# Performance work log

Hardware: AMD Instinct MI355X
Metric: run time of the kernel (lower is better)

## Reference

```python
import jax, jax.numpy as jnp
import numpy as np

N = 100000      # nodes
E = 1600000     # edges
D_IN = 64       # input feature dim
H = 64          # hidden dim
HNUM = 128      # number of direct virtual nodes (blocks)
NCONV = 2       # layers-1 conv layers in module_list
NMLP = 2        # layers-1 virtual-node MLPs (all applied each conv iter)
NEG_SLOPE = 0.2


def setup_inputs() -> dict:
    key = jax.random.key(0)
    ks = jax.random.split(key, 16)
    s = 0.1
    inp = {
        "x": jax.random.normal(ks[0], (N, D_IN), jnp.float32),
        "edge_index": jax.random.randint(ks[1], (2, E), 0, N, dtype=jnp.int32),
        "h_blocks": jax.random.randint(ks[2], (N,), 0, HNUM, dtype=jnp.int32),
        "h_levels": jax.random.randint(ks[3], (N,), 0, 4, dtype=jnp.int32),
        "h_num": HNUM,
        # initial GATConv(input->hidden): lin weight (no bias), att_src, att_dst, out bias
        "W0": jax.random.normal(ks[4], (D_IN, H), jnp.float32) * s,
        "a_src0": jax.random.normal(ks[5], (H,), jnp.float32) * s,
        "a_dst0": jax.random.normal(ks[6], (H,), jnp.float32) * s,
        "b0": jnp.zeros((H,), jnp.float32),
        # stacked module_list GATConv(hidden->hidden) params
        "Wl": jax.random.normal(ks[7], (NCONV, H, H), jnp.float32) * s,
        "a_srcl": jax.random.normal(ks[8], (NCONV, H), jnp.float32) * s,
        "a_dstl": jax.random.normal(ks[9], (NCONV, H), jnp.float32) * s,
        "bl": jnp.zeros((NCONV, H), jnp.float32),
        # virtual node embedding, torch init constant 0
        "vn_emb": jnp.zeros((1, H), jnp.float32),
        # virtual-node MLPs: Linear->ReLU->Linear->ReLU, weights stored (in,out)
        "mlp_W1": jax.random.normal(ks[10], (NMLP, H, H), jnp.float32) * s,
        "mlp_b1": jnp.zeros((NMLP, H), jnp.float32),
        "mlp_W2": jax.random.normal(ks[11], (NMLP, H, H), jnp.float32) * s,
        "mlp_b2": jnp.zeros((NMLP, H), jnp.float32),
    }
    return inp


def gat_conv(x, src, dst, W, a_src, a_dst, b, n_nodes):
    """PyG GATConv, heads=1, concat, add_self_loops=True, negative_slope=0.2."""
    h = x @ W                                    # [N, H]
    loop = jnp.arange(n_nodes, dtype=src.dtype)
    s = jnp.concatenate([src, loop])             # [E+N]
    d = jnp.concatenate([dst, loop])
    a_s = h @ a_src                              # [N]
    a_d = h @ a_dst
    e = jax.nn.leaky_relu(a_s[s] + a_d[d], negative_slope=NEG_SLOPE)  # [E+N]
    # segment softmax over destination nodes (self loops cover every segment)
    m = jax.ops.segment_max(e, d, num_segments=n_nodes)
    w = jnp.exp(e - m[d])
    denom = jax.ops.segment_sum(w, d, num_segments=n_nodes)
    alpha = w / (denom[d] + 1e-16)               # [E+N]
    out = jax.ops.segment_sum(h[s] * alpha[:, None], d, num_segments=n_nodes)
    return out + b


def reference(x, edge_index, h_blocks, h_levels, h_num,
              W0, a_src0, a_dst0, b0, Wl, a_srcl, a_dstl, bl,
              vn_emb, mlp_W1, mlp_b1, mlp_W2, mlp_b2):
    src, dst = edge_index[0], edge_index[1]
    n_nodes = x.shape[0]
    out = gat_conv(x, src, dst, W0, a_src0, a_dst0, b0, n_nodes)
    # embedding lookup of all-zero indices == broadcast of row 0
    vn_direct = jnp.broadcast_to(vn_emb[0], (h_num, vn_emb.shape[1]))  # [HNUM, H]
    vn_root = vn_emb                                                   # [1, H]
    for l in range(NCONV):
        out = out + vn_direct[h_blocks]
        out = gat_conv(out, src, dst, Wl[l], a_srcl[l], a_dstl[l], bl[l], n_nodes)
        vn_direct = jax.ops.segment_sum(out, h_blocks, num_segments=h_num) + vn_direct
        vn_direct = vn_direct + vn_root
        vn_root = jnp.sum(vn_direct, axis=0, keepdims=True) + vn_root
        # NB: the original applies EVERY vn-MLP inside each conv iteration
        for j in range(NMLP):
            vn_direct = jax.nn.relu(jax.nn.relu(vn_direct @ mlp_W1[j] + mlp_b1[j]) @ mlp_W2[j] + mlp_b2[j])
            vn_root = jax.nn.relu(jax.nn.relu(vn_root @ mlp_W1[j] + mlp_b1[j]) @ mlp_W2[j] + mlp_b2[j])
    return out
```

## Files before the change

kernel.cpp:

```cpp
#include <hip/hip_runtime.h>
#include <hip/hip_fp16.h>
#include <math.h>

#define HD 64
#define HNUM 128
#define NMLP 2
#define BSH 8
#define MAXNB 512
#define EPB 4096

typedef unsigned int uint_t;
typedef unsigned short ushort_t;
typedef _Float16 h8 __attribute__((ext_vector_type(8)));
typedef float vf4 __attribute__((ext_vector_type(4)));

union H8U { h8 v; uint_t u[4]; };

__device__ __forceinline__ float lrelu(float x){ return fmaxf(x, 0.2f*x); }

__device__ __forceinline__ float cvt_h(uint_t wv, uint_t sh){
    __half_raw hr; hr.x = (ushort_t)(wv >> sh);
    return __half2float((__half)hr);
}
__device__ __forceinline__ uint_t pk2(float a, float b){
    return (uint_t)__half_as_ushort(__float2half_rn(a)) |
           ((uint_t)__half_as_ushort(__float2half_rn(b)) << 16);
}

__global__ __launch_bounds__(256) void k_bcnt(const int* __restrict__ dst, int* __restrict__ gb,
                                              int E, int NB){
    __shared__ int h[MAXNB];
    int t = threadIdx.x;
    for(int i=t;i<NB;i+=256) h[i] = 0;
    __syncthreads();
    for(int e = blockIdx.x*256 + t; e < E; e += gridDim.x*256)
        atomicAdd(&h[dst[e]>>BSH], 1);
    __syncthreads();
    for(int i=t;i<NB;i+=256) if(h[i]) atomicAdd(&gb[i], h[i]);
}

__global__ __launch_bounds__(512) void k_bscan(const int* __restrict__ gb, int* __restrict__ bbase,
                                               int* __restrict__ gcur, int NB){
    __shared__ int s[512];
    int t = threadIdx.x;
    int v = (t < NB) ? gb[t] : 0;
    s[t] = v; __syncthreads();
    for(int o=1;o<512;o<<=1){
        int u = (t >= o) ? s[t-o] : 0;
        __syncthreads();
        s[t] += u;
        __syncthreads();
    }
    if(t < NB){ int ex = s[t] - v; bbase[t] = ex; gcur[t] = ex; }
}

__global__ __launch_bounds__(256) void k_bin(const int* __restrict__ src, const int* __restrict__ dst,
                                             int* __restrict__ gcur, uint_t* __restrict__ bdata,
                                             int E, int NB){
    __shared__ int cnt[MAXNB];
    __shared__ int base[MAXNB];
    int t = threadIdx.x;
    for(int i=t;i<NB;i+=256) cnt[i] = 0;
    __syncthreads();
    int s0 = blockIdx.x*EPB;
    uint_t pk[16]; int bk[16], off[16];
    #pragma unroll
    for(int i=0;i<16;i++){
        int e = s0 + i*256 + t;
        if(e < E){
            int sv = src[e], dv = dst[e];
            pk[i]  = ((uint_t)sv << 8) | (uint_t)(dv & 255);
            bk[i]  = dv >> BSH;
            off[i] = atomicAdd(&cnt[bk[i]], 1);
        }
    }
    __syncthreads();
    for(int i=t;i<NB;i+=256) base[i] = cnt[i] ? atomicAdd(&gcur[i], cnt[i]) : 0;
    __syncthreads();
    #pragma unroll
    for(int i=0;i<16;i++){
        int e = s0 + i*256 + t;
        if(e < E) bdata[base[bk[i]] + off[i]] = pk[i];
    }
}

__global__ __launch_bounds__(256) void k_bfuse(const uint_t* __restrict__ bdata, const int* __restrict__ bbase,
                                               const int* __restrict__ gb, int* __restrict__ rp,
                                               int* __restrict__ col, int n, int NB, int E){
    __shared__ int h[256];
    __shared__ int sc[256];
    int b = blockIdx.x, t = threadIdx.x;
    int beg = bbase[b], cnt = gb[b];
    h[t] = 0; __syncthreads();
    for(int i=t;i<cnt;i+=256) atomicAdd(&h[bdata[beg+i] & 255], 1);
    __syncthreads();
    int v = h[t];
    sc[t] = v; __syncthreads();
    for(int o=1;o<256;o<<=1){
        int u = (t >= o) ? sc[t-o] : 0;
        __syncthreads();
        sc[t] += u;
        __syncthreads();
    }
    int excl = sc[t] - v;
    int node = (b<<BSH) + t;
    if(node < n) rp[node] = beg + excl;
    if(b == NB-1 && t == 255) rp[n] = E;
    __syncthreads();
    sc[t] = excl;
    __syncthreads();
    for(int i=t;i<cnt;i+=256){
        uint_t e = bdata[beg+i];
        int pos = atomicAdd(&sc[e & 255], 1);
        col[beg + pos] = (int)(e >> 8);
    }
}

__global__ __launch_bounds__(256) void k_vcnt(const int* __restrict__ hb, int* __restrict__ vcnt, int n){
    __shared__ int h[HNUM];
    int t = threadIdx.x;
    if(t < HNUM) h[t] = 0;
    __syncthreads();
    for(int i = blockIdx.x*256 + t; i < n; i += gridDim.x*256) atomicAdd(&h[hb[i]], 1);
    __syncthreads();
    if(t < HNUM && h[t]) atomicAdd(&vcnt[t], h[t]);
}

__global__ __launch_bounds__(128) void k_vscan(const int* __restrict__ vcnt, int* __restrict__ vrp,
                                               int* __restrict__ vcur, int n){
    __shared__ int s[HNUM];
    int t = threadIdx.x;
    int v = vcnt[t];
    s[t] = v; __syncthreads();
    for(int o=1;o<HNUM;o<<=1){
        int u = (t >= o) ? s[t-o] : 0;
        __syncthreads();
        s[t] += u;
        __syncthreads();
    }
    int ex = s[t] - v;
    vrp[t] = ex; vcur[t] = ex;
    if(t == HNUM-1) vrp[HNUM] = n;
}

__global__ __launch_bounds__(256) void k_vbin(const int* __restrict__ hb, int* __restrict__ vcur,
                                              int* __restrict__ perm, int n){
    __shared__ int cnt[HNUM];
    __shared__ int base[HNUM];
    int t = threadIdx.x;
    if(t < HNUM) cnt[t] = 0;
    __syncthreads();
    int s0 = blockIdx.x*2048;
    int hv[8], off[8];
    #pragma unroll
    for(int i=0;i<8;i++){
        int nd = s0 + i*256 + t;
        if(nd < n){ hv[i] = hb[nd]; off[i] = atomicAdd(&cnt[hv[i]], 1); }
    }
    __syncthreads();
    if(t < HNUM) base[t] = cnt[t] ? atomicAdd(&vcur[t], cnt[t]) : 0;
    __syncthreads();
    #pragma unroll
    for(int i=0;i<8;i++){
        int nd = s0 + i*256 + t;
        if(nd < n) perm[base[hv[i]] + off[i]] = nd;
    }
}

__global__ __launch_bounds__(256) void k_wcvt(
    const float* __restrict__ W0, const float* __restrict__ as0, const float* __restrict__ ad0,
    const float* __restrict__ Wl, const float* __restrict__ asl, const float* __restrict__ adl,
    uint4* __restrict__ Wf3, float* __restrict__ waf3)
{
    __shared__ float wa[2][64];
    int L = blockIdx.x, t = threadIdx.x;
    const float* W  = (L==0) ? W0  : Wl  + (L-1)*HD*HD;
    const float* as = (L==0) ? as0 : asl + (L-1)*HD;
    const float* ad = (L==0) ? ad0 : adl + (L-1)*HD;
    if(t < 128){
        int sd = t>>6, k = t&63;
        const float* av = sd ? ad : as;
        float acc = 0.f;
        for(int c=0;c<HD;c++) acc = fmaf(W[k*HD+c], av[c], acc);
        wa[sd][k] = acc;
    }
    __syncthreads();
    for(int it = t; it < 512; it += 256){
        int lane = it&63, s = (it>>6)&1, tile = it>>7;
        int g = lane>>4, m = lane&15, c = tile*16 + m;
        ushort_t h[8];
        #pragma unroll
        for(int i=0;i<8;i++){
            int k = s*32 + g*4 + (i&3) + 16*(i>>2);
            h[i] = __half_as_ushort(__float2half_rn(W[k*HD + c]));
        }
        uint4 q;
        q.x = (uint_t)h[0] | ((uint_t)h[1]<<16);
        q.y = (uint_t)h[2] | ((uint_t)h[3]<<16);
        q.z = (uint_t)h[4] | ((uint_t)h[5]<<16);
        q.w = (uint_t)h[6] | ((uint_t)h[7]<<16);
        Wf3[(size_t)L*512 + (tile*2+s)*64 + lane] = q;
    }
    if(t < 128){
        int lane = t&63, sd = t>>6, g = lane>>4;
        #pragma unroll
        for(int j4=0;j4<4;j4++){
            float v[4];
            #pragma unroll
            for(int e=0;e<4;e++){
                int j = j4*4 + e;
                int k = (j>>3)*32 + g*4 + (j&3) + 16*((j>>2)&1);
                v[e] = wa[sd][k];
            }
            float* dstp = waf3 + ((size_t)L*8 + sd*4 + j4)*64*4 + lane*4;
            dstp[0]=v[0]; dstp[1]=v[1]; dstp[2]=v[2]; dstp[3]=v[3];
        }
    }
}

__global__ __launch_bounds__(256) void k_gemm(
    const float* __restrict__ IN, const float* __restrict__ addrow,
    const float* __restrict__ addtab, const int* __restrict__ hb,
    const uint4* __restrict__ Wf, const float* __restrict__ waf,
    uint_t* __restrict__ Hw, float* __restrict__ AS, float* __restrict__ AD,
    int n)
{
    __shared__ ushort_t sx[4][1024];
    int t = threadIdx.x, lane = t&63, wv = t>>6;
    int g = lane>>4, m = lane&15;
    ushort_t* sb = sx[wv];

    H8U B[8];
    #pragma unroll
    for(int f=0; f<8; f++){
        uint4 q = Wf[f*64 + lane];
        B[f].u[0]=q.x; B[f].u[1]=q.y; B[f].u[2]=q.z; B[f].u[3]=q.w;
    }
    vf4 wS[4], wD[4];
    #pragma unroll
    for(int j4=0;j4<4;j4++){
        const float* ps = waf + ((size_t)0*4 + j4)*256 + lane*4;
        const float* pd = waf + ((size_t)1*4 + j4)*256 + lane*4;
        wS[j4] = vf4{ps[0],ps[1],ps[2],ps[3]};
        wD[j4] = vf4{pd[0],pd[1],pd[2],pd[3]};
    }
    float ar0=0,ar1=0,ar2=0,ar3=0;
    if(addrow){
        const float* a = &addrow[m*4];
        ar0=a[0]; ar1=a[1]; ar2=a[2]; ar3=a[3];
    }

    int ntiles = (n + 15) >> 4;
    int wgid = (blockIdx.x*256 + t) >> 6;
    int nw = gridDim.x*4;
    for(int tile = wgid; tile < ntiles; tile += nw){
        int rb = tile*16;
        #pragma unroll
        for(int p=0;p<4;p++){
            int row = p*4 + g;
            int rowc = min(rb + row, n-1);
            float4 x4 = *(const float4*)&IN[(size_t)rowc*HD + m*4];
            if(addrow){ x4.x+=ar0; x4.y+=ar1; x4.z+=ar2; x4.w+=ar3; }
            if(addtab){
                int b = hb[rowc];
                float4 a4 = *(const float4*)&addtab[b*HD + m*4];
                x4.x+=a4.x; x4.y+=a4.y; x4.z+=a4.z; x4.w+=a4.w;
            }
            uint2 pq; pq.x = pk2(x4.x, x4.y); pq.y = pk2(x4.z, x4.w);
            int idx = (row*64 + m*4) ^ ((row&7)<<3);
            *(uint2*)&sb[idx] = pq;
        }
        int xr = (m&7)<<3;
        H8U A0, A1;
        {
            uint2 c0 = *(uint2*)&sb[(m*64 +  0 + g*4) ^ xr];
            uint2 c1 = *(uint2*)&sb[(m*64 + 16 + g*4) ^ xr];
            A0.u[0]=c0.x; A0.u[1]=c0.y; A0.u[2]=c1.x; A0.u[3]=c1.y;
            uint2 c2 = *(uint2*)&sb[(m*64 + 32 + g*4) ^ xr];
            uint2 c3 = *(uint2*)&sb[(m*64 + 48 + g*4) ^ xr];
            A1.u[0]=c2.x; A1.u[1]=c2.y; A1.u[2]=c3.x; A1.u[3]=c3.y;
        }
        float t1 = 0.f, t2 = 0.f;
        #pragma unroll
        for(int i=0;i<8;i++){
            float xv = (float)A0.v[i];
            t1 = fmaf(xv, wS[i>>2][i&3], t1);
            t2 = fmaf(xv, wD[i>>2][i&3], t2);
        }
        #pragma unroll
        for(int i=0;i<8;i++){
            float xv = (float)A1.v[i];
            t1 = fmaf(xv, wS[2+(i>>2)][i&3], t1);
            t2 = fmaf(xv, wD[2+(i>>2)][i&3], t2);
        }
        t1 += __shfl_xor(t1, 16, 64); t1 += __shfl_xor(t1, 32, 64);
        t2 += __shfl_xor(t2, 16, 64); t2 += __shfl_xor(t2, 32, 64);
        if(lane < 16 && rb + lane < n){ AS[rb+lane] = t1; AD[rb+lane] = t2; }
        vf4 z = {0.f,0.f,0.f,0.f};
        vf4 a0 = __builtin_amdgcn_mfma_f32_16x16x32_f16(A0.v, B[0].v, z, 0,0,0);
        a0     = __builtin_amdgcn_mfma_f32_16x16x32_f16(A1.v, B[1].v, a0, 0,0,0);
        vf4 a1 = __builtin_amdgcn_mfma_f32_16x16x32_f16(A0.v, B[2].v, z, 0,0,0);
        a1     = __builtin_amdgcn_mfma_f32_16x16x32_f16(A1.v, B[3].v, a1, 0,0,0);
        vf4 a2 = __builtin_amdgcn_mfma_f32_16x16x32_f16(A0.v, B[4].v, z, 0,0,0);
        a2     = __builtin_amdgcn_mfma_f32_16x16x32_f16(A1.v, B[5].v, a2, 0,0,0);
        vf4 a3 = __builtin_amdgcn_mfma_f32_16x16x32_f16(A0.v, B[6].v, z, 0,0,0);
        a3     = __builtin_amdgcn_mfma_f32_16x16x32_f16(A1.v, B[7].v, a3, 0,0,0);
        #pragma unroll
        for(int rr=0;rr<4;rr++){
            int row = rb + g*4 + rr;
            if(row < n){
                Hw[(size_t)row*32 + m]      = pk2(a0[rr], a1[rr]);
                Hw[(size_t)row*32 + 16 + m] = pk2(a2[rr], a3[rr]);
            }
        }
    }
}

__global__ __launch_bounds__(256) void k_agg(
    const uint_t* __restrict__ Hb, const float* __restrict__ AS, const float* __restrict__ AD,
    const int* __restrict__ rp, const int* __restrict__ col,
    const float* __restrict__ bias, float* __restrict__ OUT, int n)
{
    int t = threadIdx.x, lane = t & 63;
    int p = lane & 15;
    int qb = lane & 48;
    int w0 = 2*p;
    int c00 = 32*(w0>>4)+(w0&15), c01 = c00+16;
    int c10 = c00+1, c11 = c00+17;
    float b00 = bias[c00], b01 = bias[c01], b10 = bias[c10], b11 = bias[c11];
    int wv  = (blockIdx.x*256 + t) >> 6;
    int nwv = gridDim.x*4;
    for(int base = wv*4; base < n; base += nwv*4){
        int dq = min(base + (qb>>4), n-1);
        float ad = AD[dq];
        float wself = __expf(lrelu(AS[dq] + ad));
        uint2 hd = *(const uint2*)&Hb[(size_t)dq*32 + w0];
        float4 acc;
        acc.x = cvt_h(hd.x,0)*wself; acc.y = cvt_h(hd.x,16)*wself;
        acc.z = cvt_h(hd.y,0)*wself; acc.w = cvt_h(hd.y,16)*wself;
        float sacc = 0.f;
        int beg = rp[dq], end = rp[dq+1];
        int cnt = end - beg;
        int nit = (cnt + 15) >> 4;
        nit = max(nit, __shfl_xor(nit, 16, 64));
        nit = max(nit, __shfl_xor(nit, 32, 64));
        for(int it = 0; it < nit; it++){
            int j = beg + it*16 + p;
            bool valid = j < end;
            int sj = dq;
            if(cnt > 0) sj = col[valid ? j : end - 1];
            float wj = 0.f;
            if(valid) wj = __expf(lrelu(AS[sj] + ad));
            sacc += wj;
            int ccnt = cnt - it*16;
            ccnt = ccnt < 0 ? 0 : (ccnt > 16 ? 16 : ccnt);
            int emax = ccnt;
            emax = max(emax, __shfl_xor(emax, 16, 64));
            emax = max(emax, __shfl_xor(emax, 32, 64));
            int e = 0;
            for(; e + 4 <= emax; e += 4){
                float wq0 = __shfl(wj, qb+e,   64);
                float wq1 = __shfl(wj, qb+e+1, 64);
                float wq2 = __shfl(wj, qb+e+2, 64);
                float wq3 = __shfl(wj, qb+e+3, 64);
                int   sq0 = __shfl(sj, qb+e,   64);
                int   sq1 = __shfl(sj, qb+e+1, 64);
                int   sq2 = __shfl(sj, qb+e+2, 64);
                int   sq3 = __shfl(sj, qb+e+3, 64);
                uint2 v0 = *(const uint2*)&Hb[(size_t)sq0*32 + w0];
                uint2 v1 = *(const uint2*)&Hb[(size_t)sq1*32 + w0];
                uint2 v2 = *(const uint2*)&Hb[(size_t)sq2*32 + w0];
                uint2 v3 = *(const uint2*)&Hb[(size_t)sq3*32 + w0];
                acc.x = fmaf(wq0, cvt_h(v0.x,0),  acc.x);
                acc.y = fmaf(wq0, cvt_h(v0.x,16), acc.y);
                acc.z = fmaf(wq0, cvt_h(v0.y,0),  acc.z);
                acc.w = fmaf(wq0, cvt_h(v0.y,16), acc.w);
                acc.x = fmaf(wq1, cvt_h(v1.x,0),  acc.x);
                acc.y = fmaf(wq1, cvt_h(v1.x,16), acc.y);
                acc.z = fmaf(wq1, cvt_h(v1.y,0),  acc.z);
                acc.w = fmaf(wq1, cvt_h(v1.y,16), acc.w);
                acc.x = fmaf(wq2, cvt_h(v2.x,0),  acc.x);
                acc.y = fmaf(wq2, cvt_h(v2.x,16), acc.y);
                acc.z = fmaf(wq2, cvt_h(v2.y,0),  acc.z);
                acc.w = fmaf(wq2, cvt_h(v2.y,16), acc.w);
                acc.x = fmaf(wq3, cvt_h(v3.x,0),  acc.x);
                acc.y = fmaf(wq3, cvt_h(v3.x,16), acc.y);
                acc.z = fmaf(wq3, cvt_h(v3.y,0),  acc.z);
                acc.w = fmaf(wq3, cvt_h(v3.y,16), acc.w);
            }
            for(; e < emax; e++){
                float wq = __shfl(wj, qb+e, 64);
                int   sq = __shfl(sj, qb+e, 64);
                uint2 v = *(const uint2*)&Hb[(size_t)sq*32 + w0];
                acc.x = fmaf(wq, cvt_h(v.x,0),  acc.x);
                acc.y = fmaf(wq, cvt_h(v.x,16), acc.y);
                acc.z = fmaf(wq, cvt_h(v.y,0),  acc.z);
                acc.w = fmaf(wq, cvt_h(v.y,16), acc.w);
            }
        }
        sacc += __shfl_xor(sacc, 1, 64);
        sacc += __shfl_xor(sacc, 2, 64);
        sacc += __shfl_xor(sacc, 4, 64);
        sacc += __shfl_xor(sacc, 8, 64);
        float s = wself + sacc;
        float inv = 1.f/(s + 1e-16f);
        if(base + (qb>>4) < n){
            OUT[(size_t)dq*HD + c00] = fmaf(acc.x, inv, b00);
            OUT[(size_t)dq*HD + c01] = fmaf(acc.y, inv, b01);
            OUT[(size_t)dq*HD + c10] = fmaf(acc.z, inv, b10);
            OUT[(size_t)dq*HD + c11] = fmaf(acc.w, inv, b11);
        }
    }
}

__global__ __launch_bounds__(256) void k_vsum(const float* __restrict__ OUT, const int* __restrict__ perm,
                                              const int* __restrict__ vrp, float* __restrict__ vnS){
    int t = threadIdx.x, lane = t & 63, w = t >> 6;
    int g = blockIdx.x >> 3, sub = blockIdx.x & 7;
    int wig = sub*4 + w;
    int beg = vrp[g], end = vrp[g+1];
    float a0=0.f, a1=0.f, a2=0.f, a3=0.f;
    int i = beg + wig;
    for(; i + 96 < end; i += 128){
        int p0 = perm[i], p1 = perm[i+32], p2 = perm[i+64], p3 = perm[i+96];
        a0 += OUT[(size_t)p0*HD + lane];
        a1 += OUT[(size_t)p1*HD + lane];
        a2 += OUT[(size_t)p2*HD + lane];
        a3 += OUT[(size_t)p3*HD + lane];
    }
    for(; i < end; i += 32) a0 += OUT[(size_t)perm[i]*HD + lane];
    float a = (a0+a1)+(a2+a3);
    unsafeAtomicAdd(&vnS[g*HD + lane], a);
}

__global__ __launch_bounds__(64) void k_vn(
    const float* __restrict__ vnS, const float* __restrict__ vne,
    const float* __restrict__ W1, const float* __restrict__ B1,
    const float* __restrict__ W2, const float* __restrict__ B2,
    float* __restrict__ vnD)
{
    __shared__ float sx[HD];
    int lane = threadIdx.x;
    int r = blockIdx.x;
    float ve = vne[lane];
    float a = vnS[r*HD + lane] + ve + ve;
    for(int j=0;j<NMLP;j++){
        const float* w1 = W1 + j*HD*HD; const float* b1 = B1 + j*HD;
        const float* w2 = W2 + j*HD*HD; const float* b2 = B2 + j*HD;
        __syncthreads();
        sx[lane] = a;
        __syncthreads();
        float t = b1[lane];
        #pragma unroll
        for(int in=0;in<HD;in++) t = fmaf(sx[in], w1[in*HD + lane], t);
        t = fmaxf(t, 0.f);
        __syncthreads();
        sx[lane] = t;
        __syncthreads();
        float u = b2[lane];
        #pragma unroll
        for(int in=0;in<HD;in++) u = fmaf(sx[in], w2[in*HD + lane], u);
        a = fmaxf(u, 0.f);
    }
    vnD[r*HD + lane] = a;
}

extern "C" void kernel_launch(void* const* d_in, const int* in_sizes, int n_in,
                              void* d_out, int out_size, void* d_ws, size_t ws_size,
                              hipStream_t stream)
{
    const float* x   = (const float*)d_in[0];
    const int*   ei  = (const int*)d_in[1];
    const int*   hb  = (const int*)d_in[2];
    const float* W0  = (const float*)d_in[5];
    const float* as0 = (const float*)d_in[6];
    const float* ad0 = (const float*)d_in[7];
    const float* b0  = (const float*)d_in[8];
    const float* Wl  = (const float*)d_in[9];
    const float* asl = (const float*)d_in[10];
    const float* adl = (const float*)d_in[11];
    const float* bl  = (const float*)d_in[12];
    const float* vne = (const float*)d_in[13];
    const float* mW1 = (const float*)d_in[14];
    const float* mb1 = (const float*)d_in[15];
    const float* mW2 = (const float*)d_in[16];
    const float* mb2 = (const float*)d_in[17];

    int N = in_sizes[0]/HD;
    int E = in_sizes[1]/2;
    const int* src = ei;
    const int* dst = ei + E;
    int NB = (N + (1<<BSH) - 1) >> BSH;

    char* p = (char*)d_ws;
    float* f_h   = (float*)p; p += (size_t)N*HD*4;
    float* f_as  = (float*)p; p += (size_t)N*4;
    float* f_ad  = (float*)p; p += (size_t)N*4;
    float* f_vnD = (float*)p; p += HNUM*HD*4;
    float* f_vnS = (float*)p; p += HNUM*HD*4;
    int*   i_vcnt= (int*)p;   p += HNUM*4;
    int*   i_vrp = (int*)p;   p += (HNUM+1)*4;
    int*   i_vcur= (int*)p;   p += HNUM*4;
    int*   i_perm= (int*)p;   p += (size_t)N*4;
    int*   i_rp  = (int*)p;   p += (size_t)(N+1)*4;
    int*   i_gb  = (int*)p;   p += MAXNB*4;
    int*   i_bb  = (int*)p;   p += MAXNB*4;
    int*   i_gc  = (int*)p;   p += MAXNB*4;
    int*   i_col = (int*)p;   p += (size_t)E*4;
    uint4* Wf3   = (uint4*)p; p += 3*512*16;
    float* waf3  = (float*)p; p += 3*8*64*4*4;
    uint_t* bdata= (uint_t*)f_h;
    uint_t* Hw   = (uint_t*)f_h;

    float* outb = (float*)d_out;

    k_wcvt<<<3, 256, 0, stream>>>(W0, as0, ad0, Wl, asl, adl, Wf3, waf3);

    hipMemsetAsync(i_gb, 0, MAXNB*4, stream);
    hipMemsetAsync(f_vnS, 0, HNUM*HD*4 + HNUM*4, stream);
    k_bcnt <<<512, 256, 0, stream>>>(dst, i_gb, E, NB);
    k_bscan<<<1, 512, 0, stream>>>(i_gb, i_bb, i_gc, NB);
    k_bin  <<<(E+EPB-1)/EPB, 256, 0, stream>>>(src, dst, i_gc, bdata, E, NB);
    k_bfuse<<<NB, 256, 0, stream>>>(bdata, i_bb, i_gb, i_rp, i_col, N, NB, E);
    k_vcnt <<<128, 256, 0, stream>>>(hb, i_vcnt, N);
    k_vscan<<<1, 128, 0, stream>>>(i_vcnt, i_vrp, i_vcur, N);
    k_vbin <<<(N+2047)/2048, 256, 0, stream>>>(hb, i_vcur, i_perm, N);

    int ga = 4096;
    int gg = 768;
    k_gemm<<<gg, 256, 0, stream>>>(x, nullptr, nullptr, hb, Wf3, waf3, Hw, f_as, f_ad, N);
    k_agg <<<ga, 256, 0, stream>>>(Hw, f_as, f_ad, i_rp, i_col, b0, outb, N);
    k_gemm<<<gg, 256, 0, stream>>>(outb, vne, nullptr, hb, Wf3 + 512, waf3 + 2048, Hw, f_as, f_ad, N);
    k_agg <<<ga, 256, 0, stream>>>(Hw, f_as, f_ad, i_rp, i_col, bl, outb, N);
    k_vsum<<<HNUM*8, 256, 0, stream>>>(outb, i_perm, i_vrp, f_vnS);
    k_vn  <<<HNUM, 64, 0, stream>>>(f_vnS, vne, mW1, mb1, mW2, mb2, f_vnD);
    k_gemm<<<gg, 256, 0, stream>>>(outb, nullptr, f_vnD, hb, Wf3 + 1024, waf3 + 4096, Hw, f_as, f_ad, N);
    k_agg <<<ga, 256, 0, stream>>>(Hw, f_as, f_ad, i_rp, i_col, bl + HD, outb, N);
}
```

Baseline: 246.7 us.

## Process 8 destination nodes per wave with 16-byte gathers in GAT aggregation

The aggregation kernel now assigns 8 lanes per destination node instead of 16, so each lane gathers a 16-byte chunk (8 fp16 features) per neighbor rather than 8 bytes, and a wave covers 8 nodes at once. Per-edge inner loops now use each group's own edge count rather than a wave-wide maximum, and the grid is sized to cover all nodes in one pass. This is meant to cut shuffle and instruction overhead per gathered byte and widen memory transactions, at the cost of more registers per lane and more lanes in each group handling a degree-skewed edge stream.

Result: slower. 257.6 us (+4.4%).

```diff
diff --git a/kernel.cpp b/kernel.cpp
--- a/kernel.cpp
+++ b/kernel.cpp
@@ -322,93 +322,103 @@
     const float* __restrict__ bias, float* __restrict__ OUT, int n)
 {
     int t = threadIdx.x, lane = t & 63;
-    int p = lane & 15;
-    int qb = lane & 48;
-    int w0 = 2*p;
-    int c00 = 32*(w0>>4)+(w0&15), c01 = c00+16;
-    int c10 = c00+1, c11 = c00+17;
-    float b00 = bias[c00], b01 = bias[c01], b10 = bias[c10], b11 = bias[c11];
+    int p  = lane & 7;
+    int gb = lane & 56;
+    int w0 = 4*p;
+    int cc[8];
+    #pragma unroll
+    for(int k=0;k<4;k++){
+        int w = w0 + k;
+        cc[2*k]   = 32*(w>>4) + (w&15);
+        cc[2*k+1] = cc[2*k] + 16;
+    }
+    float bs[8];
+    #pragma unroll
+    for(int k=0;k<8;k++) bs[k] = bias[cc[k]];
+
     int wv  = (blockIdx.x*256 + t) >> 6;
     int nwv = gridDim.x*4;
-    for(int base = wv*4; base < n; base += nwv*4){
-        int dq = min(base + (qb>>4), n-1);
+    for(int base = wv*8; base < n; base += nwv*8){
+        int dq = min(base + (gb>>3), n-1);
         float ad = AD[dq];
         float wself = __expf(lrelu(AS[dq] + ad));
-        uint2 hd = *(const uint2*)&Hb[(size_t)dq*32 + w0];
-        float4 acc;
-        acc.x = cvt_h(hd.x,0)*wself; acc.y = cvt_h(hd.x,16)*wself;
-        acc.z = cvt_h(hd.y,0)*wself; acc.w = cvt_h(hd.y,16)*wself;
+        uint4 hd = *(const uint4*)&Hb[(size_t)dq*32 + w0];
+        float a0 = cvt_h(hd.x,0)*wself, a1 = cvt_h(hd.x,16)*wself;
+        float a2 = cvt_h(hd.y,0)*wself, a3 = cvt_h(hd.y,16)*wself;
+        float a4 = cvt_h(hd.z,0)*wself, a5 = cvt_h(hd.z,16)*wself;
+        float a6 = cvt_h(hd.w,0)*wself, a7 = cvt_h(hd.w,16)*wself;
         float sacc = 0.f;
         int beg = rp[dq], end = rp[dq+1];
         int cnt = end - beg;
-        int nit = (cnt + 15) >> 4;
+        int nit = (cnt + 7) >> 3;
+        nit = max(nit, __shfl_xor(nit, 8, 64));
         nit = max(nit, __shfl_xor(nit, 16, 64));
         nit = max(nit, __shfl_xor(nit, 32, 64));
         for(int it = 0; it < nit; it++){
-            int j = beg + it*16 + p;
+            int j = beg + it*8 + p;
             bool valid = j < end;
             int sj = dq;
             if(cnt > 0) sj = col[valid ? j : end - 1];
-            float wj = 0.f;
-            if(valid) wj = __expf(lrelu(AS[sj] + ad));
+            float wj = valid ? __expf(lrelu(AS[sj] + ad)) : 0.f;
             sacc += wj;
-            int ccnt = cnt - it*16;
-            ccnt = ccnt < 0 ? 0 : (ccnt > 16 ? 16 : ccnt);
-            int emax = ccnt;
-            emax = max(emax, __shfl_xor(emax, 16, 64));
-            emax = max(emax, __shfl_xor(emax, 32, 64));
+            int ccnt = cnt - it*8;
+            ccnt = ccnt < 0 ? 0 : (ccnt > 8 ? 8 : ccnt);
             int e = 0;
-            for(; e + 4 <= emax; e += 4){
-                float wq0 = __shfl(wj, qb+e,   64);
-                float wq1 = __shfl(wj, qb+e+1, 64);
-                float wq2 = __shfl(wj, qb+e+2, 64);
-                float wq3 = __shfl(wj, qb+e+3, 64);
-                int   sq0 = __shfl(sj, qb+e,   64);
-                int   sq1 = __shfl(sj, qb+e+1, 64);
-                int   sq2 = __shfl(sj, qb+e+2, 64);
-                int   sq3 = __shfl(sj, qb+e+3, 64);
-                uint2 v0 = *(const uint2*)&Hb[(size_t)sq0*32 + w0];
-                uint2 v1 = *(const uint2*)&Hb[(size_t)sq1*32 + w0];
-                uint2 v2 = *(const uint2*)&Hb[(size_t)sq2*32 + w0];
-                uint2 v3 = *(const uint2*)&Hb[(size_t)sq3*32 + w0];
-                acc.x = fmaf(wq0, cvt_h(v0.x,0),  acc.x);
-                acc.y = fmaf(wq0, cvt_h(v0.x,16), acc.y);
-                acc.z = fmaf(wq0, cvt_h(v0.y,0),  acc.z);
-                acc.w = fmaf(wq0, cvt_h(v0.y,16), acc.w);
-                acc.x = fmaf(wq1, cvt_h(v1.x,0),  acc.x);
-                acc.y = fmaf(wq1, cvt_h(v1.x,16), acc.y);
-                acc.z = fmaf(wq1, cvt_h(v1.y,0),  acc.z);
-                acc.w = fmaf(wq1, cvt_h(v1.y,16), acc.w);
-                acc.x = fmaf(wq2, cvt_h(v2.x,0),  acc.x);
-                acc.y = fmaf(wq2, cvt_h(v2.x,16), acc.y);
-                acc.z = fmaf(wq2, cvt_h(v2.y,0),  acc.z);
-                acc.w = fmaf(wq2, cvt_h(v2.y,16), acc.w);
-                acc.x = fmaf(wq3, cvt_h(v3.x,0),  acc.x);
-                acc.y = fmaf(wq3, cvt_h(v3.x,16), acc.y);
-                acc.z = fmaf(wq3, cvt_h(v3.y,0),  acc.z);
-                acc.w = fmaf(wq3, cvt_h(v3.y,16), acc.w);
+            for(; e + 4 <= ccnt; e += 4){
+                float wq0 = __shfl(wj, gb+e,   64);
+                float wq1 = __shfl(wj, gb+e+1, 64);
+                float wq2 = __shfl(wj, gb+e+2, 64);
+                float wq3 = __shfl(wj, gb+e+3, 64);
+                int   sq0 = __shfl(sj, gb+e,   64);
+                int   sq1 = __shfl(sj, gb+e+1, 64);
+                int   sq2 = __shfl(sj, gb+e+2, 64);
+                int   sq3 = __shfl(sj, gb+e+3, 64);
+                uint4 v0 = *(const uint4*)&Hb[(size_t)sq0*32 + w0];
+                uint4 v1 = *(const uint4*)&Hb[(size_t)sq1*32 + w0];
+                uint4 v2 = *(const uint4*)&Hb[(size_t)sq2*32 + w0];
+                uint4 v3 = *(const uint4*)&Hb[(size_t)sq3*32 + w0];
+                a0 = fmaf(wq0, cvt_h(v0.x,0),  a0); a1 = fmaf(wq0, cvt_h(v0.x,16), a1);
+                a2 = fmaf(wq0, cvt_h(v0.y,0),  a2); a3 = fmaf(wq0, cvt_h(v0.y,16), a3);
+                a4 = fmaf(wq0, cvt_h(v0.z,0),  a4); a5 = fmaf(wq0, cvt_h(v0.z,16), a5);
+                a6 = fmaf(wq0, cvt_h(v0.w,0),  a6); a7 = fmaf(wq0, cvt_h(v0.w,16), a7);
+                a0 = fmaf(wq1, cvt_h(v1.x,0),  a0); a1 = fmaf(wq1, cvt_h(v1.x,16), a1);
+                a2 = fmaf(wq1, cvt_h(v1.y,0),  a2); a3 = fmaf(wq1, cvt_h(v1.y,16), a3);
+                a4 = fmaf(wq1, cvt_h(v1.z,0),  a4); a5 = fmaf(wq1, cvt_h(v1.z,16), a5);
+                a6 = fmaf(wq1, cvt_h(v1.w,0),  a6); a7 = fmaf(wq1, cvt_h(v1.w,16), a7);
+                a0 = fmaf(wq2, cvt_h(v2.x,0),  a0); a1 = fmaf(wq2, cvt_h(v2.x,16), a1);
+                a2 = fmaf(wq2, cvt_h(v2.y,0),  a2); a3 = fmaf(wq2, cvt_h(v2.y,16), a3);
+                a4 = fmaf(wq2, cvt_h(v2.z,0),  a4); a5 = fmaf(wq2, cvt_h(v2.z,16), a5);
+                a6 = fmaf(wq2, cvt_h(v2.w,0),  a6); a7 = fmaf(wq2, cvt_h(v2.w,16), a7);
+                a0 = fmaf(wq3, cvt_h(v3.x,0),  a0); a1 = fmaf(wq3, cvt_h(v3.x,16), a1);
+                a2 = fmaf(wq3, cvt_h(v3.y,0),  a2); a3 = fmaf(wq3, cvt_h(v3.y,16), a3);
+                a4 = fmaf(wq3, cvt_h(v3.z,0),  a4); a5 = fmaf(wq3, cvt_h(v3.z,16), a5);
+                a6 = fmaf(wq3, cvt_h(v3.w,0),  a6); a7 = fmaf(wq3, cvt_h(v3.w,16), a7);
             }
-            for(; e < emax; e++){
-                float wq = __shfl(wj, qb+e, 64);
-                int   sq = __shfl(sj, qb+e, 64);
-                uint2 v = *(const uint2*)&Hb[(size_t)sq*32 + w0];
-                acc.x = fmaf(wq, cvt_h(v.x,0),  acc.x);
-                acc.y = fmaf(wq, cvt_h(v.x,16), acc.y);
-                acc.z = fmaf(wq, cvt_h(v.y,0),  acc.z);
-                acc.w = fmaf(wq, cvt_h(v.y,16), acc.w);
+            for(; e < ccnt; e++){
+                float wq = __shfl(wj, gb+e, 64);
+                int   sq = __shfl(sj, gb+e, 64);
+                uint4 v = *(const uint4*)&Hb[(size_t)sq*32 + w0];
+                a0 = fmaf(wq, cvt_h(v.x,0),  a0); a1 = fmaf(wq, cvt_h(v.x,16), a1);
+                a2 = fmaf(wq, cvt_h(v.y,0),  a2); a3 = fmaf(wq, cvt_h(v.y,16), a3);
+                a4 = fmaf(wq, cvt_h(v.z,0),  a4); a5 = fmaf(wq, cvt_h(v.z,16), a5);
+                a6 = fmaf(wq, cvt_h(v.w,0),  a6); a7 = fmaf(wq, cvt_h(v.w,16), a7);
             }
         }
         sacc += __shfl_xor(sacc, 1, 64);
         sacc += __shfl_xor(sacc, 2, 64);
         sacc += __shfl_xor(sacc, 4, 64);
-        sacc += __shfl_xor(sacc, 8, 64);
         float s = wself + sacc;
         float inv = 1.f/(s + 1e-16f);
-        if(base + (qb>>4) < n){
-            OUT[(size_t)dq*HD + c00] = fmaf(acc.x, inv, b00);
-            OUT[(size_t)dq*HD + c01] = fmaf(acc.y, inv, b01);
-            OUT[(size_t)dq*HD + c10] = fmaf(acc.z, inv, b10);
-            OUT[(size_t)dq*HD + c11] = fmaf(acc.w, inv, b11);
+        if(base + (gb>>3) < n){
+            float* orow = &OUT[(size_t)dq*HD];
+            orow[cc[0]] = fmaf(a0, inv, bs[0]);
+            orow[cc[1]] = fmaf(a1, inv, bs[1]);
+            orow[cc[2]] = fmaf(a2, inv, bs[2]);
+            orow[cc[3]] = fmaf(a3, inv, bs[3]);
+            orow[cc[4]] = fmaf(a4, inv, bs[4]);
+            orow[cc[5]] = fmaf(a5, inv, bs[5]);
+            orow[cc[6]] = fmaf(a6, inv, bs[6]);
+            orow[cc[7]] = fmaf(a7, inv, bs[7]);
         }
     }
 }
@@ -526,7 +536,7 @@
     k_vscan<<<1, 128, 0, stream>>>(i_vcnt, i_vrp, i_vcur, N);
     k_vbin <<<(N+2047)/2048, 256, 0, stream>>>(hb, i_vcur, i_perm, N);
 
-    int ga = 4096;
+    int ga = (N + 31)/32;
     int gg = 768;
     k_gemm<<<gg, 256, 0, stream>>>(x, nullptr, nullptr, hb, Wf3, waf3, Hw, f_as, f_ad, N);
     k_agg <<<ga, 256, 0, stream>>>(Hw, f_as, f_ad, i_rp, i_col, b0, outb, N);
```

## Sort destination nodes by degree to balance per-wavefront aggregation work

Applied to the files above, without the earlier changes.

Adds a counting sort of nodes by in-degree, capped at 255, built from three small kernels: histogram, scan and bin. The aggregation kernel then processes nodes in that order through a permutation array. Each wavefront handles four destination nodes and loops to the largest of their edge counts, so grouping nodes of similar degree is meant to cut idle lanes and loop-trip divergence. The cost is extra preprocessing launches and an indirection, plus the loss of sequential node order for the destination-side reads and output writes.

After: 258.7 us. 4.9% more time.

```diff
diff --git a/kernel.cpp b/kernel.cpp
--- a/kernel.cpp
+++ b/kernel.cpp
@@ -164,6 +164,60 @@
     for(int i=0;i<8;i++){
         int nd = s0 + i*256 + t;
         if(nd < n) perm[base[hv[i]] + off[i]] = nd;
+    }
+}
+
+__global__ __launch_bounds__(256) void k_dcnt(const int* __restrict__ rp, int* __restrict__ dcnt, int n){
+    __shared__ int h[256];
+    int t = threadIdx.x;
+    h[t] = 0;
+    __syncthreads();
+    for(int i = blockIdx.x*256 + t; i < n; i += gridDim.x*256){
+        int d = min(rp[i+1] - rp[i], 255);
+        atomicAdd(&h[d], 1);
+    }
+    __syncthreads();
+    if(h[t]) atomicAdd(&dcnt[t], h[t]);
+}
+
+__global__ __launch_bounds__(256) void k_dscan(const int* __restrict__ dcnt, int* __restrict__ dcur){
+    __shared__ int s[256];
+    int t = threadIdx.x;
+    int v = dcnt[t];
+    s[t] = v; __syncthreads();
+    for(int o=1;o<256;o<<=1){
+        int u = (t >= o) ? s[t-o] : 0;
+        __syncthreads();
+        s[t] += u;
+        __syncthreads();
+    }
+    dcur[t] = s[t] - v;
+}
+
+__global__ __launch_bounds__(256) void k_dbin(const int* __restrict__ rp, int* __restrict__ dcur,
+                                              int* __restrict__ dperm, int n){
+    __shared__ int cnt[256];
+    __shared__ int base[256];
+    int t = threadIdx.x;
+    cnt[t] = 0;
+    __syncthreads();
+    int s0 = blockIdx.x*2048;
+    int dv[8], off[8];
+    #pragma unroll
+    for(int i=0;i<8;i++){
+        int nd = s0 + i*256 + t;
+        if(nd < n){
+            dv[i] = min(rp[nd+1] - rp[nd], 255);
+            off[i] = atomicAdd(&cnt[dv[i]], 1);
+        }
+    }
+    __syncthreads();
+    base[t] = cnt[t] ? atomicAdd(&dcur[t], cnt[t]) : 0;
+    __syncthreads();
+    #pragma unroll
+    for(int i=0;i<8;i++){
+        int nd = s0 + i*256 + t;
+        if(nd < n) dperm[base[dv[i]] + off[i]] = nd;
     }
 }
 
@@ -318,7 +372,7 @@
 
 __global__ __launch_bounds__(256) void k_agg(
     const uint_t* __restrict__ Hb, const float* __restrict__ AS, const float* __restrict__ AD,
-    const int* __restrict__ rp, const int* __restrict__ col,
+    const int* __restrict__ rp, const int* __restrict__ col, const int* __restrict__ dperm,
     const float* __restrict__ bias, float* __restrict__ OUT, int n)
 {
     int t = threadIdx.x, lane = t & 63;
@@ -331,7 +385,8 @@
     int wv  = (blockIdx.x*256 + t) >> 6;
     int nwv = gridDim.x*4;
     for(int base = wv*4; base < n; base += nwv*4){
-        int dq = min(base + (qb>>4), n-1);
+        int pos = base + (qb>>4);
+        int dq = dperm[min(pos, n-1)];
         float ad = AD[dq];
         float wself = __expf(lrelu(AS[dq] + ad));
         uint2 hd = *(const uint2*)&Hb[(size_t)dq*32 + w0];
@@ -404,7 +459,7 @@
         sacc += __shfl_xor(sacc, 8, 64);
         float s = wself + sacc;
         float inv = 1.f/(s + 1e-16f);
-        if(base + (qb>>4) < n){
+        if(pos < n){
             OUT[(size_t)dq*HD + c00] = fmaf(acc.x, inv, b00);
             OUT[(size_t)dq*HD + c01] = fmaf(acc.y, inv, b01);
             OUT[(size_t)dq*HD + c10] = fmaf(acc.z, inv, b10);
@@ -499,9 +554,12 @@
     float* f_vnD = (float*)p; p += HNUM*HD*4;
     float* f_vnS = (float*)p; p += HNUM*HD*4;
     int*   i_vcnt= (int*)p;   p += HNUM*4;
+    int*   i_dcnt= (int*)p;   p += 256*4;
     int*   i_vrp = (int*)p;   p += (HNUM+1)*4;
     int*   i_vcur= (int*)p;   p += HNUM*4;
+    int*   i_dcur= (int*)p;   p += 256*4;
     int*   i_perm= (int*)p;   p += (size_t)N*4;
+    int*   i_dperm=(int*)p;   p += (size_t)N*4;
     int*   i_rp  = (int*)p;   p += (size_t)(N+1)*4;
     int*   i_gb  = (int*)p;   p += MAXNB*4;
     int*   i_bb  = (int*)p;   p += MAXNB*4;
@@ -517,7 +575,7 @@
     k_wcvt<<<3, 256, 0, stream>>>(W0, as0, ad0, Wl, asl, adl, Wf3, waf3);
 
     hipMemsetAsync(i_gb, 0, MAXNB*4, stream);
-    hipMemsetAsync(f_vnS, 0, HNUM*HD*4 + HNUM*4, stream);
+    hipMemsetAsync(f_vnS, 0, HNUM*HD*4 + HNUM*4 + 256*4, stream);
     k_bcnt <<<512, 256, 0, stream>>>(dst, i_gb, E, NB);
     k_bscan<<<1, 512, 0, stream>>>(i_gb, i_bb, i_gc, NB);
     k_bin  <<<(E+EPB-1)/EPB, 256, 0, stream>>>(src, dst, i_gc, bdata, E, NB);
@@ -525,15 +583,18 @@
     k_vcnt <<<128, 256, 0, stream>>>(hb, i_vcnt, N);
     k_vscan<<<1, 128, 0, stream>>>(i_vcnt, i_vrp, i_vcur, N);
     k_vbin <<<(N+2047)/2048, 256, 0, stream>>>(hb, i_vcur, i_perm, N);
+    k_dcnt <<<128, 256, 0, stream>>>(i_rp, i_dcnt, N);
+    k_dscan<<<1, 256, 0, stream>>>(i_dcnt, i_dcur);
+    k_dbin <<<(N+2047)/2048, 256, 0, stream>>>(i_rp, i_dcur, i_dperm, N);
 
     int ga = 4096;
     int gg = 768;
     k_gemm<<<gg, 256, 0, stream>>>(x, nullptr, nullptr, hb, Wf3, waf3, Hw, f_as, f_ad, N);
-    k_agg <<<ga, 256, 0, stream>>>(Hw, f_as, f_ad, i_rp, i_col, b0, outb, N);
+    k_agg <<<ga, 256, 0, stream>>>(Hw, f_as, f_ad, i_rp, i_col, i_dperm, b0, outb, N);
     k_gemm<<<gg, 256, 0, stream>>>(outb, vne, nullptr, hb, Wf3 + 512, waf3 + 2048, Hw, f_as, f_ad, N);
-    k_agg <<<ga, 256, 0, stream>>>(Hw, f_as, f_ad, i_rp, i_col, bl, outb, N);
+    k_agg <<<ga, 256, 0, stream>>>(Hw, f_as, f_ad, i_rp, i_col, i_dperm, bl, outb, N);
     k_vsum<<<HNUM*8, 256, 0, stream>>>(outb, i_perm, i_vrp, f_vnS);
     k_vn  <<<HNUM, 64, 0, stream>>>(f_vnS, vne, mW1, mb1, mW2, mb2, f_vnD);
     k_gemm<<<gg, 256, 0, stream>>>(outb, nullptr, f_vnD, hb, Wf3 + 1024, waf3 + 4096, Hw, f_as, f_ad, N);
-    k_agg <<<ga, 256, 0, stream>>>(Hw, f_as, f_ad, i_rp, i_col, bl + HD, outb, N);
-}
+    k_agg <<<ga, 256, 0, stream>>>(Hw, f_as, f_ad, i_rp, i_col, i_dperm, bl + HD, outb, N);
+}
```
